# Performance work log

Hardware: AMD Instinct MI355X
Metric: run time of the kernel (lower is better)

## Reference

```python
import jax, jax.numpy as jnp
import numpy as np

N = 50000   # nodes
F = 128     # v_feats
K = 128     # filters
H = 3       # multi_head
M = 10      # fixed neighbor count (hardcoded repeat(1,10,1) in source)


def setup_inputs() -> dict:
    key = jax.random.key(0)
    ks = jax.random.split(key, 10)
    vertices = jax.random.normal(ks[0], (N, F), jnp.float32)
    nh_indices = jax.random.randint(ks[1], (N, M), 0, N)
    int_indices = jax.random.randint(ks[2], (N, M), 0, N)
    nh_edges = jax.random.uniform(ks[3], (N, M), jnp.float32)
    int_edges = jax.random.uniform(ks[4], (N, M), jnp.float32)
    is_int = jax.random.randint(ks[5], (N,), 0, 2)
    scale = 0.05
    Wvc = jax.random.normal(ks[6], (H, F, K), jnp.float32) * scale
    Wvn_int = jax.random.normal(ks[7], (H, F, K), jnp.float32) * scale
    Wvn_nh = jax.random.normal(ks[8], (H, F, K), jnp.float32) * scale
    a = jax.random.normal(ks[9], (H, 2 * K, 1), jnp.float32) * scale
    bv = jnp.zeros((H, K), jnp.float32)
    return dict(vertices=vertices, nh_indices=nh_indices, int_indices=int_indices,
                nh_edges=nh_edges, int_edges=int_edges, is_int=is_int,
                Wvc=Wvc, bv=bv, Wvn_int=Wvn_int, Wvn_nh=Wvn_nh, a=a)


def reference(vertices, nh_indices, int_indices, nh_edges, int_edges, is_int,
              Wvc, bv, Wvn_int, Wvn_nh, a):
    n = vertices.shape[0]
    k = a.shape[1] // 2
    # Project center and neighbor features for all heads at once.
    Zc = jnp.einsum('nf,hfk->hnk', vertices, Wvc)        # [H,N,K]
    Vint = jnp.einsum('nf,hfk->hnk', vertices, Wvn_int)  # [H,N,K]
    Vnh = jnp.einsum('nf,hfk->hnk', vertices, Wvn_nh)    # [H,N,K]
    # cat((neighbor, center)) @ a  ==  neighbor @ a[:k] + center @ a[k:]
    a_n = a[:, :k, 0]  # [H,K]
    a_c = a[:, k:, 0]  # [H,K]
    e_center = jnp.einsum('hnk,hk->hn', Zc, a_c)[:, :, None]  # [H,N,1]

    def branch(Vside, idx, edges):
        mask = (idx != -1).astype(vertices.dtype)           # [N,M], -1 = pad
        g = Vside[:, idx]                                   # [H,N,M,K] gather
        e = jnp.einsum('hnmk,hk->hnm', g, a_n) + e_center   # [H,N,M]
        # faithful to source: scores zeroed (not -inf) by mask/edges before softmax
        e = e * mask[None] * edges[None]
        alpha = jax.nn.softmax(e, axis=2)                   # [H,N,M]
        norm = jnp.maximum(mask.sum(axis=1), 1.0)           # [N]
        Zn = jnp.einsum('hnmk,hnm->hnk', g * mask[None, :, :, None], alpha)
        return Zn / norm[None, :, None]

    Zn_inter = branch(Vint, int_indices, int_edges)
    Zn_chain = branch(Vnh, nh_indices, nh_edges)
    z = jax.nn.relu(Zc + Zn_inter + Zn_chain + bv[:, None, :])  # [H,N,K]
    # torch.cat(head outputs, dim=1) -> [N, H*K]
    return jnp.transpose(z, (1, 0, 2)).reshape(n, -1)
```

## Files before the change

### kernel.cpp

```cpp
#include <hip/hip_runtime.h>
#include <stdint.h>

#define N_V 50000
#define F_DIM 128
#define K_DIM 128
#define H_DIM 3
#define M_DIM 10

using bf16x8 = __attribute__((ext_vector_type(8))) short;
using f32x4  = __attribute__((ext_vector_type(4))) float;

__device__ inline unsigned short f2bf(float f) {
    union { float f; uint32_t u; } v; v.f = f;
    uint32_t u = v.u;
    u += 0x7fffu + ((u >> 16) & 1u);
    return (unsigned short)(u >> 16);
}

#define LDS_AS __attribute__((address_space(3)))
__device__ inline void gl2lds16(const void* g, void* l) {
    __builtin_amdgcn_global_load_lds(
        (const __attribute__((address_space(1))) unsigned int*)g,
        (LDS_AS unsigned int*)l, 16, 0, 0);
}

#define WTOT (9 * 128 * 128)
#define XCH  (N_V * 16)
#define WACT (9 * 128)

__global__ void prep(const float* __restrict__ Wvc,
                     const float* __restrict__ Wvn_int,
                     const float* __restrict__ Wvn_nh,
                     const float* __restrict__ X,
                     const float* __restrict__ a,
                     unsigned short* __restrict__ Wt,
                     unsigned short* __restrict__ Xb,
                     unsigned short* __restrict__ wab) {
    int idx = blockIdx.x * 256 + threadIdx.x;
    if (idx < WTOT) {
        int b   = idx >> 14;
        int rem = idx & 16383;
        int k = rem >> 7;
        int f = rem & 127;
        int h = b / 3, t = b - 3 * h;
        const float* src = (t == 0) ? Wvc : (t == 1) ? Wvn_int : Wvn_nh;
        Wt[idx] = f2bf(src[(h * 128 + f) * 128 + k]);
        return;
    }
    int xi = idx - WTOT;
    if (xi < XCH) {
        const float4* Xv = (const float4*)X;
        float4 v0 = Xv[xi * 2];
        float4 v1 = Xv[xi * 2 + 1];
        uint4 o;
        o.x = (uint32_t)f2bf(v0.x) | ((uint32_t)f2bf(v0.y) << 16);
        o.y = (uint32_t)f2bf(v0.z) | ((uint32_t)f2bf(v0.w) << 16);
        o.z = (uint32_t)f2bf(v1.x) | ((uint32_t)f2bf(v1.y) << 16);
        o.w = (uint32_t)f2bf(v1.z) | ((uint32_t)f2bf(v1.w) << 16);
        *(uint4*)&Xb[(size_t)xi * 8] = o;
        return;
    }
    int wi = xi - XCH;
    if (wi < WACT) {
        int b = wi >> 7, f = wi & 127;
        int h = b / 3, t = b - 3 * h;
        const float* src = (t == 0) ? Wvc : (t == 1) ? Wvn_int : Wvn_nh;
        const float4* wrow = (const float4*)&src[(h * 128 + f) * 128];
        const float4* av   = (const float4*)&a[h * 256 + (t == 0 ? 128 : 0)];
        float acc = 0.f;
        #pragma unroll 8
        for (int c = 0; c < 32; ++c) {
            float4 w = wrow[c], x = av[c];
            acc += w.x * x.x + w.y * x.y + w.z * x.z + w.w * x.w;
        }
        wab[b * 128 + f] = f2bf(acc);
    }
}

__global__ __launch_bounds__(256, 3) void gemm_kernel(
    const unsigned short* __restrict__ Xb,
    const unsigned short* __restrict__ Wt,
    const unsigned short* __restrict__ wab,
    float* __restrict__ out,
    uint8_t* __restrict__ Vint,
    uint8_t* __restrict__ Vnh,
    float* __restrict__ e_center,
    float* __restrict__ e_int,
    float* __restrict__ e_nh) {
    __shared__ unsigned short As[64 * 128];

    const int tid    = threadIdx.x;
    const int m_base = blockIdx.x * 64;
    const int wv     = tid >> 6;
    const int lane   = tid & 63;
    const int q      = lane >> 4;
    const int ln     = lane & 15;
    const int cb     = (wv >> 1) * 64;
    const int rb     = (wv & 1) * 32;

    #pragma unroll
    for (int it = 0; it < 4; ++it) {
        int c16 = it * 256 + tid;
        int r   = c16 >> 4;
        int p   = c16 & 15;
        int lch = p ^ (r & 15);
        int gr  = m_base + r;
        if (gr >= N_V) gr = 0;
        gl2lds16(Xb + (size_t)gr * 128 + lch * 8, &As[c16 * 8]);
    }
    __syncthreads();

    bf16x8 afr[2][4];
    #pragma unroll
    for (int rt = 0; rt < 2; ++rt) {
        int r = rb + rt * 16 + ln;
        #pragma unroll
        for (int kk = 0; kk < 4; ++kk) {
            int p = (kk * 4 + q) ^ ln;
            afr[rt][kk] = *(const bf16x8*)&As[r * 128 + p * 8];
        }
    }

    if (wv < 2) {
        bf16x8 wz[4];
        #pragma unroll
        for (int kk = 0; kk < 4; ++kk) {
            bf16x8 z = {0, 0, 0, 0, 0, 0, 0, 0};
            if (ln < 9) z = *(const bf16x8*)&wab[ln * 128 + kk * 32 + q * 8];
            wz[kk] = z;
        }
        #pragma unroll
        for (int rt = 0; rt < 2; ++rt) {
            f32x4 ae = (f32x4){0.f, 0.f, 0.f, 0.f};
            #pragma unroll
            for (int kk = 0; kk < 4; ++kk)
                ae = __builtin_amdgcn_mfma_f32_16x16x32_bf16(afr[rt][kk], wz[kk], ae, 0, 0, 0);
            if (ln < 9) {
                int hh = ln / 3, tt = ln - 3 * hh;
                float* ep = (tt == 0) ? e_center : (tt == 1) ? e_int : e_nh;
                #pragma unroll
                for (int rg = 0; rg < 4; ++rg) {
                    int gr = m_base + rb + rt * 16 + q * 4 + rg;
                    if (gr < N_V) ep[hh * N_V + gr] = ae[rg];
                }
            }
        }
    }

    const int c0 = cb + 4 * ln;
    #pragma unroll 1
    for (int b = 0; b < 9; ++b) {
        const unsigned short* Wb = Wt + (size_t)b * 16384;
        bf16x8 bfr[4][4];
        #pragma unroll
        for (int ct = 0; ct < 4; ++ct) {
            int col = cb + 4 * ln + ct;
            #pragma unroll
            for (int kk = 0; kk < 4; ++kk)
                bfr[ct][kk] = *(const bf16x8*)&Wb[col * 128 + kk * 32 + q * 8];
        }

        f32x4 acc[2][4];
        #pragma unroll
        for (int rt = 0; rt < 2; ++rt)
            #pragma unroll
            for (int ct = 0; ct < 4; ++ct) acc[rt][ct] = (f32x4){0.f, 0.f, 0.f, 0.f};

        #pragma unroll
        for (int rt = 0; rt < 2; ++rt)
            #pragma unroll
            for (int kk = 0; kk < 4; ++kk)
                #pragma unroll
                for (int ct = 0; ct < 4; ++ct)
                    acc[rt][ct] = __builtin_amdgcn_mfma_f32_16x16x32_bf16(
                        afr[rt][kk], bfr[ct][kk], acc[rt][ct], 0, 0, 0);

        int hh = b / 3;
        int tt = b - 3 * hh;
        if (tt == 0) {
            #pragma unroll
            for (int rt = 0; rt < 2; ++rt)
                #pragma unroll
                for (int rg = 0; rg < 4; ++rg) {
                    int gr = m_base + rb + rt * 16 + q * 4 + rg;
                    if (gr >= N_V) continue;
                    float4 v = make_float4(acc[rt][0][rg], acc[rt][1][rg],
                                           acc[rt][2][rg], acc[rt][3][rg]);
                    *(float4*)&out[(size_t)gr * 384 + hh * 128 + c0] = v;
                }
        } else {
            uint8_t* Vside = (tt == 1) ? Vint : Vnh;
            #pragma unroll
            for (int rt = 0; rt < 2; ++rt)
                #pragma unroll
                for (int rg = 0; rg < 4; ++rg) {
                    int gr = m_base + rb + rt * 16 + q * 4 + rg;
                    if (gr >= N_V) continue;
                    int pk = __builtin_amdgcn_cvt_pk_fp8_f32(
                        acc[rt][0][rg], acc[rt][1][rg], 0, false);
                    pk = __builtin_amdgcn_cvt_pk_fp8_f32(
                        acc[rt][2][rg], acc[rt][3][rg], pk, true);
                    *(uint32_t*)&Vside[((size_t)(hh * N_V + gr)) * 128 + c0] =
                        (uint32_t)pk;
                }
        }
    }
}

__global__ __launch_bounds__(256) void attn_kernel(
    const int* __restrict__ nh_idx, const int* __restrict__ int_idx,
    const float* __restrict__ nh_edge, const float* __restrict__ int_edge,
    const float* __restrict__ bv,
    const uint8_t* __restrict__ Vint,
    const uint8_t* __restrict__ Vnh,
    const float* __restrict__ ec, const float* __restrict__ ei,
    const float* __restrict__ en,
    float* __restrict__ out) {
    const int wv   = threadIdx.x >> 6;
    const int lane = threadIdx.x & 63;
    const int n    = blockIdx.x * 4 + wv;
    if (n >= N_V) return;
    const int g  = lane >> 4;
    const int gl = lane & 15;

    const bool part = (g <= 1) && (gl < M_DIM);
    int jm = -1; float wm = 0.f;
    if (part) {
        const int*   idx = (g == 0) ? int_idx  : nh_idx;
        const float* ed  = (g == 0) ? int_edge : nh_edge;
        jm = idx[n * M_DIM + gl];
        wm = ed[n * M_DIM + gl];
    }
    const bool  valid = part && (jm >= 0);
    const int   jc    = valid ? jm : 0;
    const float vfl   = valid ? 1.f : 0.f;

    float cf = vfl;
    #pragma unroll
    for (int off = 1; off < 16; off <<= 1) cf += __shfl_xor(cf, off, 64);
    const float cnorm = fmaxf(cf, 1.f);

    const int src_base = (g < 2 ? 0 : 16) + (g & 1) * 5;
    int jrow[5];
    #pragma unroll
    for (int i = 0; i < 5; ++i) jrow[i] = __shfl(jc, src_base + i, 64);

    for (int h = 0; h < H_DIM; ++h) {
        const float ecv = ec[h * N_V + n];

        float l = -3.0e38f;
        if (part) {
            const float* es = (g == 0) ? ei : en;
            float e = es[h * N_V + jc];
            l = valid ? (e + ecv) * wm : 0.f;
        }
        float mx = l;
        #pragma unroll
        for (int off = 1; off < 16; off <<= 1) mx = fmaxf(mx, __shfl_xor(mx, off, 64));
        float ex = part ? __expf(l - mx) : 0.f;
        float sv = ex;
        #pragma unroll
        for (int off = 1; off < 16; off <<= 1) sv += __shfl_xor(sv, off, 64);
        float alphap = valid ? ex / (sv * cnorm) : 0.f;

        const uint8_t* Vb = ((g < 2) ? Vint : Vnh) + (size_t)h * N_V * 128;
        float acc[8] = {0.f, 0.f, 0.f, 0.f, 0.f, 0.f, 0.f, 0.f};
        #pragma unroll
        for (int i = 0; i < 5; ++i) {
            float al  = __shfl(alphap, src_base + i, 64);
            uint2 pv  = *(const uint2*)&Vb[(size_t)jrow[i] * 128 + gl * 8];
            auto f01 = __builtin_amdgcn_cvt_pk_f32_fp8(pv.x, false);
            auto f23 = __builtin_amdgcn_cvt_pk_f32_fp8(pv.x, true);
            auto f45 = __builtin_amdgcn_cvt_pk_f32_fp8(pv.y, false);
            auto f67 = __builtin_amdgcn_cvt_pk_f32_fp8(pv.y, true);
            acc[0] += al * f01[0];
            acc[1] += al * f01[1];
            acc[2] += al * f23[0];
            acc[3] += al * f23[1];
            acc[4] += al * f45[0];
            acc[5] += al * f45[1];
            acc[6] += al * f67[0];
            acc[7] += al * f67[1];
        }
        #pragma unroll
        for (int c = 0; c < 8; ++c) {
            acc[c] += __shfl_xor(acc[c], 16, 64);
            acc[c] += __shfl_xor(acc[c], 32, 64);
        }
        if (g < 2) {
            size_t o = (size_t)n * 384 + h * 128 + gl * 8 + g * 4;
            float4 zc = *(const float4*)&out[o];
            float4 bb = *(const float4*)&bv[h * 128 + gl * 8 + g * 4];
            float4 zn;
            if (g == 0) zn = make_float4(acc[0], acc[1], acc[2], acc[3]);
            else        zn = make_float4(acc[4], acc[5], acc[6], acc[7]);
            float4 r;
            r.x = fmaxf(zc.x + zn.x + bb.x, 0.f);
            r.y = fmaxf(zc.y + zn.y + bb.y, 0.f);
            r.z = fmaxf(zc.z + zn.z + bb.z, 0.f);
            r.w = fmaxf(zc.w + zn.w + bb.w, 0.f);
            *(float4*)&out[o] = r;
        }
    }
}

extern "C" void kernel_launch(void* const* d_in, const int* in_sizes, int n_in,
                              void* d_out, int out_size, void* d_ws, size_t ws_size,
                              hipStream_t stream) {
    const float* vertices    = (const float*)d_in[0];
    const int*   nh_indices  = (const int*)d_in[1];
    const int*   int_indices = (const int*)d_in[2];
    const float* nh_edges    = (const float*)d_in[3];
    const float* int_edges   = (const float*)d_in[4];
    const float* Wvc     = (const float*)d_in[6];
    const float* bv      = (const float*)d_in[7];
    const float* Wvn_int = (const float*)d_in[8];
    const float* Wvn_nh  = (const float*)d_in[9];
    const float* a       = (const float*)d_in[10];
    float* out = (float*)d_out;

    char* ws = (char*)d_ws;
    size_t off = 0;
    unsigned short* Wt = (unsigned short*)(ws + off);
    off += (size_t)WTOT * 2;                  off = (off + 255) & ~(size_t)255;
    unsigned short* wab = (unsigned short*)(ws + off);
    off += (size_t)WACT * 2;                  off = (off + 255) & ~(size_t)255;
    unsigned short* Xb = (unsigned short*)(ws + off);
    off += (size_t)N_V * 128 * 2;             off = (off + 255) & ~(size_t)255;
    uint8_t* Vint = (uint8_t*)(ws + off);
    off += (size_t)H_DIM * N_V * 128;         off = (off + 255) & ~(size_t)255;
    uint8_t* Vnh = (uint8_t*)(ws + off);
    off += (size_t)H_DIM * N_V * 128;         off = (off + 255) & ~(size_t)255;
    float* e_center = (float*)(ws + off);
    off += (size_t)H_DIM * N_V * 4;           off = (off + 255) & ~(size_t)255;
    float* e_int = (float*)(ws + off);
    off += (size_t)H_DIM * N_V * 4;           off = (off + 255) & ~(size_t)255;
    float* e_nh = (float*)(ws + off);
    off += (size_t)H_DIM * N_V * 4;

    int prep_threads = WTOT + XCH + WACT;
    prep<<<(prep_threads + 255) / 256, 256, 0, stream>>>(
        Wvc, Wvn_int, Wvn_nh, vertices, a, Wt, Xb, wab);

    dim3 grid_g((N_V + 63) / 64);
    gemm_kernel<<<grid_g, 256, 0, stream>>>(Xb, Wt, wab, out, Vint, Vnh,
                                            e_center, e_int, e_nh);

    attn_kernel<<<(N_V + 3) / 4, 256, 0, stream>>>(
        nh_indices, int_indices, nh_edges, int_edges, bv,
        Vint, Vnh, e_center, e_int, e_nh, out);
}
```

Measured before the change: 275.4 us.

## Split GEMM grid by weight block with double-buffered row tiles; hoist attention gathers

New measurement: 246.1 us. -10.6%, faster.

```diff
diff --git a/kernel.cpp b/kernel.cpp
--- a/kernel.cpp
+++ b/kernel.cpp
@@ -6,6 +6,7 @@
 #define K_DIM 128
 #define H_DIM 3
 #define M_DIM 10
+#define TILES_PER_BLK 4
 
 using bf16x8 = __attribute__((ext_vector_type(8))) short;
 using f32x4  = __attribute__((ext_vector_type(4))) float;
@@ -84,80 +85,78 @@
     float* __restrict__ out,
     uint8_t* __restrict__ Vint,
     uint8_t* __restrict__ Vnh,
-    float* __restrict__ e_center,
-    float* __restrict__ e_int,
-    float* __restrict__ e_nh) {
-    __shared__ unsigned short As[64 * 128];
-
-    const int tid    = threadIdx.x;
-    const int m_base = blockIdx.x * 64;
-    const int wv     = tid >> 6;
-    const int lane   = tid & 63;
-    const int q      = lane >> 4;
-    const int ln     = lane & 15;
-    const int cb     = (wv >> 1) * 64;
-    const int rb     = (wv & 1) * 32;
-
-    #pragma unroll
-    for (int it = 0; it < 4; ++it) {
-        int c16 = it * 256 + tid;
-        int r   = c16 >> 4;
-        int p   = c16 & 15;
-        int lch = p ^ (r & 15);
-        int gr  = m_base + r;
-        if (gr >= N_V) gr = 0;
-        gl2lds16(Xb + (size_t)gr * 128 + lch * 8, &As[c16 * 8]);
-    }
-    __syncthreads();
-
-    bf16x8 afr[2][4];
-    #pragma unroll
-    for (int rt = 0; rt < 2; ++rt) {
-        int r = rb + rt * 16 + ln;
-        #pragma unroll
-        for (int kk = 0; kk < 4; ++kk) {
-            int p = (kk * 4 + q) ^ ln;
-            afr[rt][kk] = *(const bf16x8*)&As[r * 128 + p * 8];
-        }
-    }
-
-    if (wv < 2) {
-        bf16x8 wz[4];
+    float* __restrict__ ec4,
+    float* __restrict__ ei4,
+    float* __restrict__ en4) {
+    __shared__ unsigned short As[2][64 * 128];
+
+    const int tid  = threadIdx.x;
+    const int b    = blockIdx.y;
+    const int hh   = b / 3;
+    const int tt   = b - 3 * hh;
+    const int wv   = tid >> 6;
+    const int lane = tid & 63;
+    const int q    = lane >> 4;
+    const int ln   = lane & 15;
+    const int cb   = (wv >> 1) * 64;
+    const int rb   = (wv & 1) * 32;
+    const int m0   = blockIdx.x * (64 * TILES_PER_BLK);
+
+    auto stage = [&](int buf, int tile) {
+        const int mb = m0 + tile * 64;
+        #pragma unroll
+        for (int it = 0; it < 4; ++it) {
+            int c16 = it * 256 + tid;
+            int r   = c16 >> 4;
+            int p   = c16 & 15;
+            int lch = p ^ (r & 15);
+            int gr  = mb + r;
+            if (gr >= N_V) gr = 0;
+            gl2lds16(Xb + (size_t)gr * 128 + lch * 8, &As[buf][c16 * 8]);
+        }
+    };
+
+    stage(0, 0);
+
+    const unsigned short* Wb = Wt + (size_t)b * 16384;
+    bf16x8 bfr[4][4];
+    #pragma unroll
+    for (int ct = 0; ct < 4; ++ct) {
+        int col = cb + 4 * ln + ct;
+        #pragma unroll
+        for (int kk = 0; kk < 4; ++kk)
+            bfr[ct][kk] = *(const bf16x8*)&Wb[col * 128 + kk * 32 + q * 8];
+    }
+
+    const bool do_e = (b == 0) && (wv < 2);
+    bf16x8 wz[4];
+    if (do_e) {
         #pragma unroll
         for (int kk = 0; kk < 4; ++kk) {
             bf16x8 z = {0, 0, 0, 0, 0, 0, 0, 0};
             if (ln < 9) z = *(const bf16x8*)&wab[ln * 128 + kk * 32 + q * 8];
             wz[kk] = z;
         }
+    }
+
+    __syncthreads();
+
+    const int c0 = cb + 4 * ln;
+    #pragma unroll
+    for (int t = 0; t < TILES_PER_BLK; ++t) {
+        const int mb = m0 + t * 64;
+
+        if (t + 1 < TILES_PER_BLK) stage((t + 1) & 1, t + 1);
+
+        bf16x8 afr[2][4];
         #pragma unroll
         for (int rt = 0; rt < 2; ++rt) {
-            f32x4 ae = (f32x4){0.f, 0.f, 0.f, 0.f};
-            #pragma unroll
-            for (int kk = 0; kk < 4; ++kk)
-                ae = __builtin_amdgcn_mfma_f32_16x16x32_bf16(afr[rt][kk], wz[kk], ae, 0, 0, 0);
-            if (ln < 9) {
-                int hh = ln / 3, tt = ln - 3 * hh;
-                float* ep = (tt == 0) ? e_center : (tt == 1) ? e_int : e_nh;
-                #pragma unroll
-                for (int rg = 0; rg < 4; ++rg) {
-                    int gr = m_base + rb + rt * 16 + q * 4 + rg;
-                    if (gr < N_V) ep[hh * N_V + gr] = ae[rg];
-                }
+            int r = rb + rt * 16 + ln;
+            #pragma unroll
+            for (int kk = 0; kk < 4; ++kk) {
+                int p = (kk * 4 + q) ^ ln;
+                afr[rt][kk] = *(const bf16x8*)&As[t & 1][r * 128 + p * 8];
             }
-        }
-    }
-
-    const int c0 = cb + 4 * ln;
-    #pragma unroll 1
-    for (int b = 0; b < 9; ++b) {
-        const unsigned short* Wb = Wt + (size_t)b * 16384;
-        bf16x8 bfr[4][4];
-        #pragma unroll
-        for (int ct = 0; ct < 4; ++ct) {
-            int col = cb + 4 * ln + ct;
-            #pragma unroll
-            for (int kk = 0; kk < 4; ++kk)
-                bfr[ct][kk] = *(const bf16x8*)&Wb[col * 128 + kk * 32 + q * 8];
         }
 
         f32x4 acc[2][4];
@@ -175,14 +174,34 @@
                     acc[rt][ct] = __builtin_amdgcn_mfma_f32_16x16x32_bf16(
                         afr[rt][kk], bfr[ct][kk], acc[rt][ct], 0, 0, 0);
 
-        int hh = b / 3;
-        int tt = b - 3 * hh;
+        if (do_e) {
+            #pragma unroll
+            for (int rt = 0; rt < 2; ++rt) {
+                f32x4 ae = (f32x4){0.f, 0.f, 0.f, 0.f};
+                #pragma unroll
+                for (int kk = 0; kk < 4; ++kk)
+                    ae = __builtin_amdgcn_mfma_f32_16x16x32_bf16(
+                        afr[rt][kk], wz[kk], ae, 0, 0, 0);
+                if (ln < 9) {
+                    int h2 = ln / 3, t2 = ln - 3 * h2;
+                    float* ep = (t2 == 0) ? ec4 : (t2 == 1) ? ei4 : en4;
+                    #pragma unroll
+                    for (int rg = 0; rg < 4; ++rg) {
+                        int gr = mb + rb + rt * 16 + q * 4 + rg;
+                        if (gr < N_V) ep[gr * 4 + h2] = ae[rg];
+                    }
+                }
+            }
+        }
+
+        __syncthreads();
+
         if (tt == 0) {
             #pragma unroll
             for (int rt = 0; rt < 2; ++rt)
                 #pragma unroll
                 for (int rg = 0; rg < 4; ++rg) {
-                    int gr = m_base + rb + rt * 16 + q * 4 + rg;
+                    int gr = mb + rb + rt * 16 + q * 4 + rg;
                     if (gr >= N_V) continue;
                     float4 v = make_float4(acc[rt][0][rg], acc[rt][1][rg],
                                            acc[rt][2][rg], acc[rt][3][rg]);
@@ -194,7 +213,7 @@
             for (int rt = 0; rt < 2; ++rt)
                 #pragma unroll
                 for (int rg = 0; rg < 4; ++rg) {
-                    int gr = m_base + rb + rt * 16 + q * 4 + rg;
+                    int gr = mb + rb + rt * 16 + q * 4 + rg;
                     if (gr >= N_V) continue;
                     int pk = __builtin_amdgcn_cvt_pk_fp8_f32(
                         acc[rt][0][rg], acc[rt][1][rg], 0, false);
@@ -213,8 +232,8 @@
     const float* __restrict__ bv,
     const uint8_t* __restrict__ Vint,
     const uint8_t* __restrict__ Vnh,
-    const float* __restrict__ ec, const float* __restrict__ ei,
-    const float* __restrict__ en,
+    const float* __restrict__ ec4, const float* __restrict__ ei4,
+    const float* __restrict__ en4,
     float* __restrict__ out) {
     const int wv   = threadIdx.x >> 6;
     const int lane = threadIdx.x & 63;
@@ -245,15 +264,34 @@
     #pragma unroll
     for (int i = 0; i < 5; ++i) jrow[i] = __shfl(jc, src_base + i, 64);
 
+    uint2 pv[3][5];
+    #pragma unroll
     for (int h = 0; h < H_DIM; ++h) {
-        const float ecv = ec[h * N_V + n];
+        const uint8_t* Vb = ((g < 2) ? Vint : Vnh) + (size_t)h * N_V * 128;
+        #pragma unroll
+        for (int i = 0; i < 5; ++i)
+            pv[h][i] = *(const uint2*)&Vb[(size_t)jrow[i] * 128 + gl * 8];
+    }
+    float4 ev = make_float4(0.f, 0.f, 0.f, 0.f);
+    if (part) ev = *(const float4*)&(((g == 0) ? ei4 : en4)[jc * 4]);
+    const float4 ecv = *(const float4*)&ec4[n * 4];
+
+    float4 zc[3], bb[3];
+    if (g < 2) {
+        #pragma unroll
+        for (int h = 0; h < H_DIM; ++h) {
+            zc[h] = *(const float4*)&out[(size_t)n * 384 + h * 128 + gl * 8 + g * 4];
+            bb[h] = *(const float4*)&bv[h * 128 + gl * 8 + g * 4];
+        }
+    }
+
+    #pragma unroll
+    for (int h = 0; h < H_DIM; ++h) {
+        const float eh  = (h == 0) ? ev.x  : (h == 1) ? ev.y  : ev.z;
+        const float ech = (h == 0) ? ecv.x : (h == 1) ? ecv.y : ecv.z;
 
         float l = -3.0e38f;
-        if (part) {
-            const float* es = (g == 0) ? ei : en;
-            float e = es[h * N_V + jc];
-            l = valid ? (e + ecv) * wm : 0.f;
-        }
+        if (part) l = valid ? (eh + ech) * wm : 0.f;
         float mx = l;
         #pragma unroll
         for (int off = 1; off < 16; off <<= 1) mx = fmaxf(mx, __shfl_xor(mx, off, 64));
@@ -263,16 +301,15 @@
         for (int off = 1; off < 16; off <<= 1) sv += __shfl_xor(sv, off, 64);
         float alphap = valid ? ex / (sv * cnorm) : 0.f;
 
-        const uint8_t* Vb = ((g < 2) ? Vint : Vnh) + (size_t)h * N_V * 128;
         float acc[8] = {0.f, 0.f, 0.f, 0.f, 0.f, 0.f, 0.f, 0.f};
         #pragma unroll
         for (int i = 0; i < 5; ++i) {
-            float al  = __shfl(alphap, src_base + i, 64);
-            uint2 pv  = *(const uint2*)&Vb[(size_t)jrow[i] * 128 + gl * 8];
-            auto f01 = __builtin_amdgcn_cvt_pk_f32_fp8(pv.x, false);
-            auto f23 = __builtin_amdgcn_cvt_pk_f32_fp8(pv.x, true);
-            auto f45 = __builtin_amdgcn_cvt_pk_f32_fp8(pv.y, false);
-            auto f67 = __builtin_amdgcn_cvt_pk_f32_fp8(pv.y, true);
+            float al = __shfl(alphap, src_base + i, 64);
+            uint2 p  = pv[h][i];
+            auto f01 = __builtin_amdgcn_cvt_pk_f32_fp8(p.x, false);
+            auto f23 = __builtin_amdgcn_cvt_pk_f32_fp8(p.x, true);
+            auto f45 = __builtin_amdgcn_cvt_pk_f32_fp8(p.y, false);
+            auto f67 = __builtin_amdgcn_cvt_pk_f32_fp8(p.y, true);
             acc[0] += al * f01[0];
             acc[1] += al * f01[1];
             acc[2] += al * f23[0];
@@ -289,16 +326,14 @@
         }
         if (g < 2) {
             size_t o = (size_t)n * 384 + h * 128 + gl * 8 + g * 4;
-            float4 zc = *(const float4*)&out[o];
-            float4 bb = *(const float4*)&bv[h * 128 + gl * 8 + g * 4];
             float4 zn;
             if (g == 0) zn = make_float4(acc[0], acc[1], acc[2], acc[3]);
             else        zn = make_float4(acc[4], acc[5], acc[6], acc[7]);
             float4 r;
-            r.x = fmaxf(zc.x + zn.x + bb.x, 0.f);
-            r.y = fmaxf(zc.y + zn.y + bb.y, 0.f);
-            r.z = fmaxf(zc.z + zn.z + bb.z, 0.f);
-            r.w = fmaxf(zc.w + zn.w + bb.w, 0.f);
+            r.x = fmaxf(zc[h].x + zn.x + bb[h].x, 0.f);
+            r.y = fmaxf(zc[h].y + zn.y + bb[h].y, 0.f);
+            r.z = fmaxf(zc[h].z + zn.z + bb[h].z, 0.f);
+            r.w = fmaxf(zc[h].w + zn.w + bb[h].w, 0.f);
             *(float4*)&out[o] = r;
         }
     }
@@ -331,22 +366,22 @@
     off += (size_t)H_DIM * N_V * 128;         off = (off + 255) & ~(size_t)255;
     uint8_t* Vnh = (uint8_t*)(ws + off);
     off += (size_t)H_DIM * N_V * 128;         off = (off + 255) & ~(size_t)255;
-    float* e_center = (float*)(ws + off);
-    off += (size_t)H_DIM * N_V * 4;           off = (off + 255) & ~(size_t)255;
-    float* e_int = (float*)(ws + off);
-    off += (size_t)H_DIM * N_V * 4;           off = (off + 255) & ~(size_t)255;
-    float* e_nh = (float*)(ws + off);
-    off += (size_t)H_DIM * N_V * 4;
+    float* ec4 = (float*)(ws + off);
+    off += (size_t)N_V * 4 * 4;               off = (off + 255) & ~(size_t)255;
+    float* ei4 = (float*)(ws + off);
+    off += (size_t)N_V * 4 * 4;               off = (off + 255) & ~(size_t)255;
+    float* en4 = (float*)(ws + off);
+    off += (size_t)N_V * 4 * 4;
 
     int prep_threads = WTOT + XCH + WACT;
     prep<<<(prep_threads + 255) / 256, 256, 0, stream>>>(
         Wvc, Wvn_int, Wvn_nh, vertices, a, Wt, Xb, wab);
 
-    dim3 grid_g((N_V + 63) / 64);
+    dim3 grid_g((N_V + 64 * TILES_PER_BLK - 1) / (64 * TILES_PER_BLK), 9);
     gemm_kernel<<<grid_g, 256, 0, stream>>>(Xb, Wt, wab, out, Vint, Vnh,
-                                            e_center, e_int, e_nh);
+                                            ec4, ei4, en4);
 
     attn_kernel<<<(N_V + 3) / 4, 256, 0, stream>>>(
         nh_indices, int_indices, nh_edges, int_edges, bv,
-        Vint, Vnh, e_center, e_int, e_nh, out);
-}
+        Vint, Vnh, ec4, ei4, en4, out);
+}
```
